# Kernel optimization log

Hardware: AMD Instinct MI355X
Metric: run time of the kernel (lower is better)

Reference implementation:

```python
import jax, jax.numpy as jnp
import numpy as np

NUM_HEADS = 8
NUM_NEIGHBORS = 32


def setup_inputs() -> dict:
    key = jax.random.key(0)
    ks = jax.random.split(key, 5)
    B, S, F, C = 4, 2048, 512, 3
    x = jax.random.normal(ks[0], (B, S, F), dtype=jnp.float32)
    coords = jax.random.uniform(ks[1], (B, S, C), dtype=jnp.float32)
    scale = 1.0 / np.sqrt(F)
    Wq = jax.random.normal(ks[2], (F, F), dtype=jnp.float32) * scale
    Wk = jax.random.normal(ks[3], (F, F), dtype=jnp.float32) * scale
    Wv = jax.random.normal(ks[4], (F, F), dtype=jnp.float32) * scale
    return {"x": x, "coords": coords, "Wq": Wq, "Wk": Wk, "Wv": Wv}


def _nearest_neighbors(coords, k):
    # coords: [B,S,C] -> dists [B,S,S]; drop self (index 0 after argsort)
    diff = coords[:, None, :, :] - coords[:, :, None, :]
    dists = jnp.linalg.norm(diff, axis=-1)
    return jnp.argsort(dists, axis=-1)[:, :, 1:k + 1]  # [B,S,K]


def reference(x, coords, Wq, Wk, Wv):
    B, S, F = x.shape
    H = NUM_HEADS
    D = F // H

    nn_idx = _nearest_neighbors(coords, NUM_NEIGHBORS)  # [B,S,K] int
    # dense boolean neighbor mask [B,S,S]: mask[b,q,kv] = kv in nn_idx[b,q]
    b_ix = jnp.arange(B)[:, None, None]
    q_ix = jnp.arange(S)[None, :, None]
    mask = jnp.zeros((B, S, S), dtype=bool).at[b_ix, q_ix, nn_idx].set(True)

    q = (x @ Wq.T).reshape(B, S, H, D).transpose(0, 2, 1, 3)  # [B,H,S,D]
    k = (x @ Wk.T).reshape(B, S, H, D).transpose(0, 2, 1, 3)
    v = (x @ Wv.T).reshape(B, S, H, D).transpose(0, 2, 1, 3)

    scale = 1.0 / jnp.sqrt(jnp.asarray(D, dtype=x.dtype))
    scores = jnp.einsum("bhqd,bhkd->bhqk", q, k) * scale
    neg_inf = jnp.asarray(-jnp.inf, dtype=scores.dtype)
    scores = jnp.where(mask[:, None, :, :], scores, neg_inf)
    attn = jax.nn.softmax(scores, axis=-1)
    out = jnp.einsum("bhqk,bhkd->bhqd", attn, v)  # [B,H,S,D]
    out = out.transpose(0, 2, 1, 3).reshape(B, S, F)
    metric = k.mean(axis=2)  # [B,H,D]
    return out, metric
```

## Files before the change

kernel.cpp:

```cpp
#include <hip/hip_runtime.h>
#include <stdint.h>

#define BATCH 4
#define SEQ   2048
#define FDIM  512
#define NHEAD 8
#define HDIM  64
#define KNN   32

typedef unsigned int u32;
typedef unsigned long long u64;
typedef unsigned short u16;
typedef unsigned short bf16_t;

typedef __attribute__((ext_vector_type(8))) short short8;
typedef __attribute__((ext_vector_type(4))) float f32x4;

#define SF  ((size_t)SEQ * FDIM)
#define BSF ((size_t)BATCH * SF)

#define CAST_NB 2432
#define XPART_NB 128

__device__ __forceinline__ bf16_t f2bf(float f) {
    u32 x = __float_as_uint(f);
    return (bf16_t)((x + 0x7FFFu + ((x >> 16) & 1u)) >> 16);
}
__device__ __forceinline__ float bf2f(bf16_t u) { return __uint_as_float(((u32)u) << 16); }
__device__ __forceinline__ void bf2x2(u32 p, float& a, float& b) {
    a = __uint_as_float(p << 16);
    b = __uint_as_float(p & 0xFFFF0000u);
}
__device__ __forceinline__ u64 min_u64(u64 a, u64 b) { return a < b ? a : b; }
__device__ __forceinline__ u64 shfl_xor_u64(u64 v, int m) {
    int lo = __shfl_xor((int)(u32)v, m, 64);
    int hi = __shfl_xor((int)(u32)(v >> 32), m, 64);
    return (((u64)(u32)hi) << 32) | (u32)lo;
}

__device__ __forceinline__ void cast_body(int cid,
                                          const float* __restrict__ x,
                                          const float* __restrict__ wq,
                                          const float* __restrict__ wk,
                                          const float* __restrict__ wv,
                                          bf16_t* __restrict__ xb,
                                          bf16_t* __restrict__ wqb,
                                          bf16_t* __restrict__ wkb,
                                          bf16_t* __restrict__ wvb) {
    int z, blk;
    if (cid < 2048) { z = 0; blk = cid; }
    else { int d = cid - 2048; z = 1 + (d >> 7); blk = d & 127; }
    const float* src = (z == 0) ? x : (z == 1) ? wq : (z == 2) ? wk : wv;
    bf16_t* dst      = (z == 0) ? xb : (z == 1) ? wqb : (z == 2) ? wkb : wvb;
    size_t idx = (size_t)blk * 256 + threadIdx.x;
    const float4 a = ((const float4*)src)[idx * 2 + 0];
    const float4 b = ((const float4*)src)[idx * 2 + 1];
    uint4 o;
    o.x = (u32)f2bf(a.x) | ((u32)f2bf(a.y) << 16);
    o.y = (u32)f2bf(a.z) | ((u32)f2bf(a.w) << 16);
    o.z = (u32)f2bf(b.x) | ((u32)f2bf(b.y) << 16);
    o.w = (u32)f2bf(b.z) | ((u32)f2bf(b.w) << 16);
    ((uint4*)dst)[idx] = o;
}

__device__ __forceinline__ void xpart_body(int id, const float* __restrict__ x,
                                           float* __restrict__ xpart) {
    const int b = id >> 5, chunk = id & 31;
    const int tid = threadIdx.x;
    const float* xp = x + (size_t)b * SF + (size_t)chunk * 64 * FDIM;
    float s0 = 0.f, s1 = 0.f;
    for (int r = 0; r < 64; ++r) {
        s0 += xp[(size_t)r * FDIM + tid];
        s1 += xp[(size_t)r * FDIM + tid + 256];
    }
    float* dst = xpart + (size_t)id * FDIM;
    dst[tid]       = s0 * (1.f / 2048.f);
    dst[tid + 256] = s1 * (1.f / 2048.f);
}

__device__ __forceinline__ void knn_body(char* smem, int blk,
                                         const float* __restrict__ coords,
                                         u16* __restrict__ nn_out) {
    u32* chist = (u32*)smem;
    u32* fhist = (u32*)(smem + 256);
    u64* bk    = (u64*)(smem + 1280);
    u64* wpart = (u64*)(smem + 1792);
    u32* sc    = (u32*)(smem + 1824);
    const int b   = blk >> 11;
    const int qi  = blk & (SEQ - 1);
    const int t   = threadIdx.x;
    const int wid = t >> 6, lane = t & 63;
    const size_t qb = (size_t)blk * KNN;

    fhist[t & 255] = 0;
    if (t < 64) chist[t] = 0;
    if (t == 0) { sc[2] = 0; sc[3] = 0; }

    const float* cb = coords + (size_t)b * SEQ * 3;
    const float qx = cb[qi * 3 + 0];
    const float qy = cb[qi * 3 + 1];
    const float qz = cb[qi * 3 + 2];

    float dist[8];
    int   ib[8];
    u64 tmin = ~0ull;
#pragma unroll
    for (int i = 0; i < 8; ++i) {
        int c = i * 256 + t;
        float dx = __fsub_rn(cb[c * 3 + 0], qx);
        float dy = __fsub_rn(cb[c * 3 + 1], qy);
        float dz = __fsub_rn(cb[c * 3 + 2], qz);
        float d2 = __fadd_rn(__fadd_rn(__fmul_rn(dx, dx), __fmul_rn(dy, dy)),
                             __fmul_rn(dz, dz));
        dist[i] = __fsqrt_rn(d2);
        ib[i] = (int)(dist[i] * 8192.0f);
        u64 key = (((u64)__float_as_uint(dist[i])) << 32) | (u32)c;
        tmin = min_u64(tmin, key);
    }
    tmin = min_u64(tmin, shfl_xor_u64(tmin, 1));
    tmin = min_u64(tmin, shfl_xor_u64(tmin, 2));
    tmin = min_u64(tmin, shfl_xor_u64(tmin, 4));
    tmin = min_u64(tmin, shfl_xor_u64(tmin, 8));
    tmin = min_u64(tmin, shfl_xor_u64(tmin, 16));
    tmin = min_u64(tmin, shfl_xor_u64(tmin, 32));
    if (lane == 0) wpart[wid] = tmin;
    __syncthreads();

#pragma unroll
    for (int i = 0; i < 8; ++i) atomicAdd(&chist[ib[i] >> 8], 1u);
    const u64 M = min_u64(min_u64(wpart[0], wpart[1]),
                          min_u64(wpart[2], wpart[3]));
    __syncthreads();

    if (t < 64) {
        u32 h = chist[t];
        u32 cum = h;
#pragma unroll
        for (int d = 1; d < 64; d <<= 1) {
            u32 v = (u32)__shfl_up((int)cum, d, 64);
            if (t >= d) cum += v;
        }
        u64 bal = __ballot(cum >= 33);
        int Bc = __ffsll((long long)bal) - 1;
        u32 excl = cum - h;
        u32 base = (u32)__shfl((int)excl, Bc, 64);
        if (t == 0) { sc[0] = (u32)Bc; sc[1] = base; }
    }
    __syncthreads();

    {
        const int Bc = (int)sc[0];
#pragma unroll
        for (int i = 0; i < 8; ++i)
            if ((ib[i] >> 8) == Bc) atomicAdd(&fhist[ib[i] & 255], 1u);
    }
    __syncthreads();

    if (t < 64) {
        const u32 Bc = sc[0], base = sc[1];
        u32 f0 = fhist[t * 4 + 0], f1 = fhist[t * 4 + 1];
        u32 f2 = fhist[t * 4 + 2], f3 = fhist[t * 4 + 3];
        u32 s = f0 + f1 + f2 + f3;
        u32 cum = s;
#pragma unroll
        for (int d = 1; d < 64; d <<= 1) {
            u32 v = (u32)__shfl_up((int)cum, d, 64);
            if (t >= d) cum += v;
        }
        u32 E = base + (cum - s);
        u32 c0 = E + f0, c1 = c0 + f1, c2 = c1 + f2, c3 = c2 + f3;
        u64 bal = __ballot(c3 >= 33);
        int L = __ffsll((long long)bal) - 1;
        if (t == L) {
            int j = (c0 >= 33) ? 0 : (c1 >= 33) ? 1 : (c2 >= 33) ? 2 : 3;
            sc[4] = (Bc << 8) | (u32)(t * 4 + j);
        }
    }
    __syncthreads();

    {
        const int ibt = (int)sc[4];
#pragma unroll
        for (int i = 0; i < 8; ++i) {
            int c = i * 256 + t;
            u64 key = (((u64)__float_as_uint(dist[i])) << 32) | (u32)c;
            if (ib[i] < ibt) {
                if (key != M) {
                    u32 pos = atomicAdd(&sc[2], 1u);
                    nn_out[qb + pos] = (u16)c;
                }
            } else if (ib[i] == ibt) {
                u32 bp = atomicAdd(&sc[3], 1u);
                if (bp < 64) bk[bp] = key;
            }
        }
    }
    __syncthreads();

    if (t < 64) {
        const u32 m = sc[2];
        const int n = (int)min(sc[3], 64u);
        const int need = 32 - (int)m;
        u64 k = (t < n) ? bk[t] : ~0ull;
        if (k == M) k = ~0ull;
#pragma unroll 1
        for (int r = 0; r < need; ++r) {
            u64 g = k;
            g = min_u64(g, shfl_xor_u64(g, 1));
            g = min_u64(g, shfl_xor_u64(g, 2));
            g = min_u64(g, shfl_xor_u64(g, 4));
            g = min_u64(g, shfl_xor_u64(g, 8));
            g = min_u64(g, shfl_xor_u64(g, 16));
            g = min_u64(g, shfl_xor_u64(g, 32));
            if (k == g) {
                nn_out[qb + m + r] = (u16)(g & 0x7FF);
                k = ~0ull;
            }
        }
    }
}

__global__ __launch_bounds__(256) void fused_ck(const float* __restrict__ x,
                                                const float* __restrict__ wq,
                                                const float* __restrict__ wk,
                                                const float* __restrict__ wv,
                                                bf16_t* __restrict__ xb,
                                                bf16_t* __restrict__ wqb,
                                                bf16_t* __restrict__ wkb,
                                                bf16_t* __restrict__ wvb,
                                                const float* __restrict__ coords,
                                                u16* __restrict__ nn_out,
                                                float* __restrict__ xpart) {
    __shared__ __align__(16) char smem[1856];
    const int bid = blockIdx.x;
    if (bid < CAST_NB) {
        cast_body(bid, x, wq, wk, wv, xb, wqb, wkb, wvb);
    } else if (bid < CAST_NB + XPART_NB) {
        xpart_body(bid - CAST_NB, x, xpart);
    } else {
        knn_body(smem, bid - CAST_NB - XPART_NB, coords, nn_out);
    }
}

__global__ __launch_bounds__(256) void gemm_mfma(const bf16_t* __restrict__ xb,
                                                 const bf16_t* __restrict__ wqb,
                                                 const bf16_t* __restrict__ wkb,
                                                 const bf16_t* __restrict__ wvb,
                                                 float* __restrict__ qout,
                                                 bf16_t* __restrict__ kvout,
                                                 const float* __restrict__ xpart,
                                                 const float* __restrict__ Wkf,
                                                 float* __restrict__ metric) {
    __shared__ __align__(16) bf16_t As[128 * 32];
    __shared__ __align__(16) bf16_t Bs[128 * 32];
    const int z = blockIdx.z;
    const int tid  = threadIdx.x;

    if (z == 3) {
        const int id = blockIdx.y * 4 + blockIdx.x;
        if (id >= 8) return;
        float* xbarL = (float*)As;
        const int b = id >> 1;
        float a0 = 0.f, a1 = 0.f;
#pragma unroll 4
        for (int c = 0; c < 32; ++c) {
            const float* xp = xpart + (size_t)((b << 5) | c) * FDIM;
            a0 += xp[tid];
            a1 += xp[tid + 256];
        }
        xbarL[tid] = a0; xbarL[tid + 256] = a1;
        __syncthreads();
        const int f = ((id & 1) << 8) | tid;
        const float* wr = Wkf + (size_t)f * FDIM;
        float acc = 0.f;
#pragma unroll 4
        for (int kk = 0; kk < FDIM; kk += 4) {
            float4 wv = *(const float4*)(wr + kk);
            acc += xbarL[kk + 0] * wv.x + xbarL[kk + 1] * wv.y
                 + xbarL[kk + 2] * wv.z + xbarL[kk + 3] * wv.w;
        }
        metric[(b << 9) | f] = acc;
        return;
    }

    const bf16_t* W = (z == 0) ? wqb : (z == 1) ? wkb : wvb;
    const int wid  = tid >> 6, lane = tid & 63;
    const int m16  = lane & 15, quad = lane >> 4;
    const int wm   = (wid & 1) * 64;
    const int wn   = (wid >> 1) * 64;
    const int m0   = blockIdx.y * 128;
    const int n0   = blockIdx.x * 128;

    const int sr = tid >> 2, sc = (tid & 3) * 8;
    const bf16_t* agp = xb + (size_t)(m0 + sr) * FDIM + sc;
    const bf16_t* bgp = W  + (size_t)(n0 + sr) * FDIM + sc;

    f32x4 acc[4][4];
#pragma unroll
    for (int i = 0; i < 4; ++i)
#pragma unroll
        for (int j = 0; j < 4; ++j) acc[i][j] = (f32x4){0.f, 0.f, 0.f, 0.f};

#pragma unroll 1
    for (int k0 = 0; k0 < FDIM; k0 += 32) {
        uint4 a0 = *(const uint4*)(agp + k0);
        uint4 a1 = *(const uint4*)(agp + (size_t)64 * FDIM + k0);
        uint4 b0 = *(const uint4*)(bgp + k0);
        uint4 b1 = *(const uint4*)(bgp + (size_t)64 * FDIM + k0);
        __syncthreads();
        *(uint4*)(As + sr * 32 + sc)        = a0;
        *(uint4*)(As + (sr + 64) * 32 + sc) = a1;
        *(uint4*)(Bs + sr * 32 + sc)        = b0;
        *(uint4*)(Bs + (sr + 64) * 32 + sc) = b1;
        __syncthreads();

        short8 af[4], bfr[4];
#pragma unroll
        for (int i = 0; i < 4; ++i)
            af[i] = *(const short8*)(As + (wm + i * 16 + m16) * 32 + quad * 8);
#pragma unroll
        for (int j = 0; j < 4; ++j)
            bfr[j] = *(const short8*)(Bs + (wn + j * 16 + m16) * 32 + quad * 8);
#pragma unroll
        for (int i = 0; i < 4; ++i)
#pragma unroll
            for (int j = 0; j < 4; ++j)
                acc[i][j] = __builtin_amdgcn_mfma_f32_16x16x32_bf16(af[i], bfr[j],
                                                                    acc[i][j], 0, 0, 0);
    }

    if (z == 0) {
#pragma unroll
        for (int i = 0; i < 4; ++i) {
            const int rowb = m0 + wm + i * 16 + quad * 4;
#pragma unroll
            for (int r = 0; r < 4; ++r) {
                float* orow = qout + (size_t)(rowb + r) * FDIM + n0 + wn + m16;
                orow[ 0] = acc[i][0][r]; orow[16] = acc[i][1][r];
                orow[32] = acc[i][2][r]; orow[48] = acc[i][3][r];
            }
        }
    } else {
        bf16_t* base = kvout + (size_t)(z - 1) * BSF;
#pragma unroll
        for (int i = 0; i < 4; ++i) {
            const int rowb = m0 + wm + i * 16 + quad * 4;
#pragma unroll
            for (int r = 0; r < 4; ++r) {
                bf16_t* orow = base + (size_t)(rowb + r) * FDIM + n0 + wn + m16;
                orow[ 0] = f2bf(acc[i][0][r]); orow[16] = f2bf(acc[i][1][r]);
                orow[32] = f2bf(acc[i][2][r]); orow[48] = f2bf(acc[i][3][r]);
            }
        }
    }
}

__global__ __launch_bounds__(256, 8) void attn_kernel(const bf16_t* __restrict__ kv,
                                                      const u16* __restrict__ nn,
                                                      float* __restrict__ out) {
    __shared__ float qsl[4][64];
    const int i   = blockIdx.x;
    const int b   = (i & 7) >> 1;
    const int jb  = ((i >> 3) << 1) | (i & 1);
    const int tid = threadIdx.x;
    const int wid = tid >> 6, lane = tid & 63;
    const int gid = (jb << 2) | wid;
    const int qi  = gid >> 3, h = gid & 7;
    const int blk = (b << 11) | qi;

    int sreg = 0;
    if (lane < KNN) sreg = (int)nn[(size_t)blk * KNN + lane] & (SEQ - 1);
    qsl[wid][lane] = out[(size_t)blk * FDIM + h * HDIM + lane];
    __asm__ volatile("s_waitcnt lgkmcnt(0)" ::: "memory");
    __builtin_amdgcn_wave_barrier();

    const int j = lane & 31, half = lane >> 5;
    const int rowj = __shfl(sreg, j, 64);
    const bf16_t* kreg = kv + ((size_t)((b << 11) + rowj)) * FDIM + h * HDIM + half * 32;
    uint4 k0 = *(const uint4*)(kreg + 0);
    uint4 k1 = *(const uint4*)(kreg + 8);
    uint4 k2 = *(const uint4*)(kreg + 16);
    uint4 k3 = *(const uint4*)(kreg + 24);

    const int g = lane >> 4, l = lane & 15;
    const bf16_t* vbase = kv + BSF + ((size_t)(b << 11)) * FDIM + h * HDIM + l * 4;
    uint2 vv[8];
#pragma unroll
    for (int t2 = 0; t2 < 8; ++t2) {
        const int row = __shfl(sreg, (g << 3) | t2, 64);
        vv[t2] = *(const uint2*)(vbase + (size_t)row * FDIM);
    }

    const float* qp = &qsl[wid][half * 32];
    float acc = 0.f;
    {
        float f0, f1, f2, f3, f4, f5, f6, f7;
        bf2x2(k0.x, f0, f1); bf2x2(k0.y, f2, f3);
        bf2x2(k0.z, f4, f5); bf2x2(k0.w, f6, f7);
        acc += qp[0] * f0 + qp[1] * f1 + qp[2] * f2 + qp[3] * f3
             + qp[4] * f4 + qp[5] * f5 + qp[6] * f6 + qp[7] * f7;
        bf2x2(k1.x, f0, f1); bf2x2(k1.y, f2, f3);
        bf2x2(k1.z, f4, f5); bf2x2(k1.w, f6, f7);
        acc += qp[8] * f0 + qp[9] * f1 + qp[10] * f2 + qp[11] * f3
             + qp[12] * f4 + qp[13] * f5 + qp[14] * f6 + qp[15] * f7;
        bf2x2(k2.x, f0, f1); bf2x2(k2.y, f2, f3);
        bf2x2(k2.z, f4, f5); bf2x2(k2.w, f6, f7);
        acc += qp[16] * f0 + qp[17] * f1 + qp[18] * f2 + qp[19] * f3
             + qp[20] * f4 + qp[21] * f5 + qp[22] * f6 + qp[23] * f7;
        bf2x2(k3.x, f0, f1); bf2x2(k3.y, f2, f3);
        bf2x2(k3.z, f4, f5); bf2x2(k3.w, f6, f7);
        acc += qp[24] * f0 + qp[25] * f1 + qp[26] * f2 + qp[27] * f3
             + qp[28] * f4 + qp[29] * f5 + qp[30] * f6 + qp[31] * f7;
    }
    acc += __shfl_xor(acc, 32, 64);
    float s = acc * 0.125f;
    float m = s;
    m = fmaxf(m, __shfl_xor(m, 1, 64));
    m = fmaxf(m, __shfl_xor(m, 2, 64));
    m = fmaxf(m, __shfl_xor(m, 4, 64));
    m = fmaxf(m, __shfl_xor(m, 8, 64));
    m = fmaxf(m, __shfl_xor(m, 16, 64));
    float e = __expf(s - m);
    float sum = e;
    sum += __shfl_xor(sum, 1, 64);
    sum += __shfl_xor(sum, 2, 64);
    sum += __shfl_xor(sum, 4, 64);
    sum += __shfl_xor(sum, 8, 64);
    sum += __shfl_xor(sum, 16, 64);
    float w = e / sum;

    float o0 = 0.f, o1 = 0.f, o2 = 0.f, o3 = 0.f;
#pragma unroll
    for (int t2 = 0; t2 < 8; ++t2) {
        const float wj = __shfl(w, (g << 3) | t2, 64);
        float f0, f1, f2, f3;
        bf2x2(vv[t2].x, f0, f1); bf2x2(vv[t2].y, f2, f3);
        o0 += wj * f0; o1 += wj * f1; o2 += wj * f2; o3 += wj * f3;
    }
    o0 += __shfl_xor(o0, 16, 64); o0 += __shfl_xor(o0, 32, 64);
    o1 += __shfl_xor(o1, 16, 64); o1 += __shfl_xor(o1, 32, 64);
    o2 += __shfl_xor(o2, 16, 64); o2 += __shfl_xor(o2, 32, 64);
    o3 += __shfl_xor(o3, 16, 64); o3 += __shfl_xor(o3, 32, 64);
    if (g == 0) {
        float4 ov = make_float4(o0, o1, o2, o3);
        *(float4*)(out + (size_t)blk * FDIM + h * HDIM + l * 4) = ov;
    }
}

extern "C" void kernel_launch(void* const* d_in, const int* in_sizes, int n_in,
                              void* d_out, int out_size, void* d_ws, size_t ws_size,
                              hipStream_t stream) {
    const float* x      = (const float*)d_in[0];
    const float* coords = (const float*)d_in[1];
    const float* Wq     = (const float*)d_in[2];
    const float* Wk     = (const float*)d_in[3];
    const float* Wv     = (const float*)d_in[4];
    float* out    = (float*)d_out;
    float* metric = out + BSF;

    char* p = (char*)d_ws;
    bf16_t* xb    = (bf16_t*)p;                      p += BSF * sizeof(bf16_t);
    bf16_t* wqb   = (bf16_t*)p;                      p += (size_t)FDIM * FDIM * sizeof(bf16_t);
    bf16_t* wkb   = (bf16_t*)p;                      p += (size_t)FDIM * FDIM * sizeof(bf16_t);
    bf16_t* wvb   = (bf16_t*)p;                      p += (size_t)FDIM * FDIM * sizeof(bf16_t);
    bf16_t* kv    = (bf16_t*)p;                      p += 2 * BSF * sizeof(bf16_t);
    u16*    nn    = (u16*)p;                         p += (size_t)BATCH * SEQ * KNN * sizeof(u16);
    float*  xpart = (float*)p;

    fused_ck<<<CAST_NB + XPART_NB + BATCH * SEQ, 256, 0, stream>>>(
        x, Wq, Wk, Wv, xb, wqb, wkb, wvb, coords, nn, xpart);

    gemm_mfma<<<dim3(FDIM / 128, (BATCH * SEQ) / 128, 4), 256, 0, stream>>>(
        xb, wqb, wkb, wvb, out, kv, xpart, Wk, metric);

    attn_kernel<<<BATCH * SEQ * NHEAD / 4, 256, 0, stream>>>(kv, nn, out);
}
```

Measured before the change: 184.3 us.

## Store Q as bf16 and use packed bf16 dot2 plus DPP reductions in attention

The projection epilogue now writes Q as bf16 into the fp32 output buffer, laid out with a per-head stride so each head's 64 values sit in the first half of its slot. The attention kernel loads Q as packed u32 pairs and computes QK dot products with the fdot2 bf16 builtin in two accumulator chains. It also replaces the intra-16-lane shuffles in the softmax max and sum reductions with DPP row operations. This lowers Q write/read traffic and ALU work, but Q is rounded to bf16 and the reduction depends on the DPP control codes being correct.

New measurement: 189.7 us. +2.9%, slower.

```diff
diff --git a/kernel.cpp b/kernel.cpp
--- a/kernel.cpp
+++ b/kernel.cpp
@@ -15,6 +15,7 @@
 
 typedef __attribute__((ext_vector_type(8))) short short8;
 typedef __attribute__((ext_vector_type(4))) float f32x4;
+typedef __attribute__((ext_vector_type(2))) __bf16 bf16x2;
 
 #define SF  ((size_t)SEQ * FDIM)
 #define BSF ((size_t)BATCH * SF)
@@ -36,6 +37,23 @@
     int lo = __shfl_xor((int)(u32)v, m, 64);
     int hi = __shfl_xor((int)(u32)(v >> 32), m, 64);
     return (((u64)(u32)hi) << 32) | (u32)lo;
+}
+
+__device__ __forceinline__ float dot2bf(u32 a, u32 b, float c) {
+#if __has_builtin(__builtin_amdgcn_fdot2_f32_bf16)
+    return __builtin_amdgcn_fdot2_f32_bf16(__builtin_bit_cast(bf16x2, a),
+                                           __builtin_bit_cast(bf16x2, b), c, false);
+#else
+    float a0, a1, b0, b1;
+    bf2x2(a, a0, a1); bf2x2(b, b0, b1);
+    return c + a0 * b0 + a1 * b1;
+#endif
+}
+
+template <int CTRL>
+__device__ __forceinline__ float dppf(float x) {
+    return __int_as_float(__builtin_amdgcn_update_dpp(
+        0, __float_as_int(x), CTRL, 0xF, 0xF, true));
 }
 
 __device__ __forceinline__ void cast_body(int cid,
@@ -330,14 +348,18 @@
     }
 
     if (z == 0) {
+        u16* qb16 = (u16*)qout;
 #pragma unroll
         for (int i = 0; i < 4; ++i) {
             const int rowb = m0 + wm + i * 16 + quad * 4;
 #pragma unroll
             for (int r = 0; r < 4; ++r) {
-                float* orow = qout + (size_t)(rowb + r) * FDIM + n0 + wn + m16;
-                orow[ 0] = acc[i][0][r]; orow[16] = acc[i][1][r];
-                orow[32] = acc[i][2][r]; orow[48] = acc[i][3][r];
+                u16* orow = qb16 + (size_t)(rowb + r) * (2 * FDIM);
+#pragma unroll
+                for (int jj = 0; jj < 4; ++jj) {
+                    const int col = n0 + wn + m16 + jj * 16;
+                    orow[((col >> 6) << 7) + (col & 63)] = f2bf(acc[i][jj][r]);
+                }
             }
         }
     } else {
@@ -358,7 +380,7 @@
 __global__ __launch_bounds__(256, 8) void attn_kernel(const bf16_t* __restrict__ kv,
                                                       const u16* __restrict__ nn,
                                                       float* __restrict__ out) {
-    __shared__ float qsl[4][64];
+    __shared__ __align__(16) u32 qslu[4][32];
     const int i   = blockIdx.x;
     const int b   = (i & 7) >> 1;
     const int jb  = ((i >> 3) << 1) | (i & 1);
@@ -369,8 +391,10 @@
     const int blk = (b << 11) | qi;
 
     int sreg = 0;
-    if (lane < KNN) sreg = (int)nn[(size_t)blk * KNN + lane] & (SEQ - 1);
-    qsl[wid][lane] = out[(size_t)blk * FDIM + h * HDIM + lane];
+    if (lane < 32) {
+        sreg = (int)nn[(size_t)blk * KNN + lane] & (SEQ - 1);
+        qslu[wid][lane] = ((const u32*)out)[(size_t)blk * FDIM + h * HDIM + lane];
+    }
     __asm__ volatile("s_waitcnt lgkmcnt(0)" ::: "memory");
     __builtin_amdgcn_wave_barrier();
 
@@ -391,41 +415,32 @@
         vv[t2] = *(const uint2*)(vbase + (size_t)row * FDIM);
     }
 
-    const float* qp = &qsl[wid][half * 32];
-    float acc = 0.f;
-    {
-        float f0, f1, f2, f3, f4, f5, f6, f7;
-        bf2x2(k0.x, f0, f1); bf2x2(k0.y, f2, f3);
-        bf2x2(k0.z, f4, f5); bf2x2(k0.w, f6, f7);
-        acc += qp[0] * f0 + qp[1] * f1 + qp[2] * f2 + qp[3] * f3
-             + qp[4] * f4 + qp[5] * f5 + qp[6] * f6 + qp[7] * f7;
-        bf2x2(k1.x, f0, f1); bf2x2(k1.y, f2, f3);
-        bf2x2(k1.z, f4, f5); bf2x2(k1.w, f6, f7);
-        acc += qp[8] * f0 + qp[9] * f1 + qp[10] * f2 + qp[11] * f3
-             + qp[12] * f4 + qp[13] * f5 + qp[14] * f6 + qp[15] * f7;
-        bf2x2(k2.x, f0, f1); bf2x2(k2.y, f2, f3);
-        bf2x2(k2.z, f4, f5); bf2x2(k2.w, f6, f7);
-        acc += qp[16] * f0 + qp[17] * f1 + qp[18] * f2 + qp[19] * f3
-             + qp[20] * f4 + qp[21] * f5 + qp[22] * f6 + qp[23] * f7;
-        bf2x2(k3.x, f0, f1); bf2x2(k3.y, f2, f3);
-        bf2x2(k3.z, f4, f5); bf2x2(k3.w, f6, f7);
-        acc += qp[24] * f0 + qp[25] * f1 + qp[26] * f2 + qp[27] * f3
-             + qp[28] * f4 + qp[29] * f5 + qp[30] * f6 + qp[31] * f7;
-    }
+    const u32* qp = &qslu[wid][half * 16];
+    float a0 = 0.f, a1 = 0.f;
+    a0 = dot2bf(qp[0],  k0.x, a0); a1 = dot2bf(qp[1],  k0.y, a1);
+    a0 = dot2bf(qp[2],  k0.z, a0); a1 = dot2bf(qp[3],  k0.w, a1);
+    a0 = dot2bf(qp[4],  k1.x, a0); a1 = dot2bf(qp[5],  k1.y, a1);
+    a0 = dot2bf(qp[6],  k1.z, a0); a1 = dot2bf(qp[7],  k1.w, a1);
+    a0 = dot2bf(qp[8],  k2.x, a0); a1 = dot2bf(qp[9],  k2.y, a1);
+    a0 = dot2bf(qp[10], k2.z, a0); a1 = dot2bf(qp[11], k2.w, a1);
+    a0 = dot2bf(qp[12], k3.x, a0); a1 = dot2bf(qp[13], k3.y, a1);
+    a0 = dot2bf(qp[14], k3.z, a0); a1 = dot2bf(qp[15], k3.w, a1);
+    float acc = a0 + a1;
     acc += __shfl_xor(acc, 32, 64);
     float s = acc * 0.125f;
+
     float m = s;
-    m = fmaxf(m, __shfl_xor(m, 1, 64));
-    m = fmaxf(m, __shfl_xor(m, 2, 64));
-    m = fmaxf(m, __shfl_xor(m, 4, 64));
-    m = fmaxf(m, __shfl_xor(m, 8, 64));
+    m = fmaxf(m, dppf<0xB1>(m));
+    m = fmaxf(m, dppf<0x4E>(m));
+    m = fmaxf(m, dppf<0x141>(m));
+    m = fmaxf(m, dppf<0x140>(m));
     m = fmaxf(m, __shfl_xor(m, 16, 64));
     float e = __expf(s - m);
     float sum = e;
-    sum += __shfl_xor(sum, 1, 64);
-    sum += __shfl_xor(sum, 2, 64);
-    sum += __shfl_xor(sum, 4, 64);
-    sum += __shfl_xor(sum, 8, 64);
+    sum += dppf<0xB1>(sum);
+    sum += dppf<0x4E>(sum);
+    sum += dppf<0x141>(sum);
+    sum += dppf<0x140>(sum);
     sum += __shfl_xor(sum, 16, 64);
     float w = e / sum;
 
```

## Remap attention lanes to 8-lane groups with DPP reductions and LDS output sum

Applied to the files above, without the earlier changes.

Rearranges the per-(query,head) attention wave so each lane holds 8 contiguous dims of 4 neighbors for both K and V, loaded as 16-byte vectors issued together up front. Dot-product partials are reduced with DPP row operations instead of a cross-half shuffle, and softmax max/sum use fewer shuffles. The output is reduced across the 8 neighbor groups through a shared-memory buffer instead of shuffle trees. In exchange it uses more LDS and registers, and the occupancy hint drops from 8 to 6.

New measurement: 163.0 us. 11.5% less time.

```diff
diff --git a/kernel.cpp b/kernel.cpp
--- a/kernel.cpp
+++ b/kernel.cpp
@@ -36,6 +36,28 @@
     int lo = __shfl_xor((int)(u32)v, m, 64);
     int hi = __shfl_xor((int)(u32)(v >> 32), m, 64);
     return (((u64)(u32)hi) << 32) | (u32)lo;
+}
+
+template <int CTRL>
+__device__ __forceinline__ float dppf(float x) {
+    return __int_as_float(__builtin_amdgcn_update_dpp(
+        0, __float_as_int(x), CTRL, 0xF, 0xF, true));
+}
+
+__device__ __forceinline__ float dot8(uint4 k, f32x4 qa, f32x4 qb) {
+    float f0, f1, f2, f3, f4, f5, f6, f7;
+    bf2x2(k.x, f0, f1); bf2x2(k.y, f2, f3);
+    bf2x2(k.z, f4, f5); bf2x2(k.w, f6, f7);
+    return qa.x * f0 + qa.y * f1 + qa.z * f2 + qa.w * f3
+         + qb.x * f4 + qb.y * f5 + qb.z * f6 + qb.w * f7;
+}
+
+__device__ __forceinline__ void acc8(uint4 v, float w, float* o) {
+    float f0, f1, f2, f3, f4, f5, f6, f7;
+    bf2x2(v.x, f0, f1); bf2x2(v.y, f2, f3);
+    bf2x2(v.z, f4, f5); bf2x2(v.w, f6, f7);
+    o[0] += w * f0; o[1] += w * f1; o[2] += w * f2; o[3] += w * f3;
+    o[4] += w * f4; o[5] += w * f5; o[6] += w * f6; o[7] += w * f7;
 }
 
 __device__ __forceinline__ void cast_body(int cid,
@@ -355,10 +377,11 @@
     }
 }
 
-__global__ __launch_bounds__(256, 8) void attn_kernel(const bf16_t* __restrict__ kv,
+__global__ __launch_bounds__(256, 6) void attn_kernel(const bf16_t* __restrict__ kv,
                                                       const u16* __restrict__ nn,
                                                       float* __restrict__ out) {
     __shared__ float qsl[4][64];
+    __shared__ float osl[4][8][64];
     const int i   = blockIdx.x;
     const int b   = (i & 7) >> 1;
     const int jb  = ((i >> 3) << 1) | (i & 1);
@@ -371,80 +394,65 @@
     int sreg = 0;
     if (lane < KNN) sreg = (int)nn[(size_t)blk * KNN + lane] & (SEQ - 1);
     qsl[wid][lane] = out[(size_t)blk * FDIM + h * HDIM + lane];
+
+    const int g3 = lane >> 3, l8 = lane & 7;
+    const int r0 = __shfl(sreg,      g3, 64);
+    const int r1 = __shfl(sreg,  8 + g3, 64);
+    const int r2 = __shfl(sreg, 16 + g3, 64);
+    const int r3 = __shfl(sreg, 24 + g3, 64);
+
+    const bf16_t* base = kv + ((size_t)(b << 11)) * FDIM + h * HDIM + l8 * 8;
+    const uint4 k0 = *(const uint4*)(base + (size_t)r0 * FDIM);
+    const uint4 k1 = *(const uint4*)(base + (size_t)r1 * FDIM);
+    const uint4 k2 = *(const uint4*)(base + (size_t)r2 * FDIM);
+    const uint4 k3 = *(const uint4*)(base + (size_t)r3 * FDIM);
+    const uint4 v0 = *(const uint4*)(base + BSF + (size_t)r0 * FDIM);
+    const uint4 v1 = *(const uint4*)(base + BSF + (size_t)r1 * FDIM);
+    const uint4 v2 = *(const uint4*)(base + BSF + (size_t)r2 * FDIM);
+    const uint4 v3 = *(const uint4*)(base + BSF + (size_t)r3 * FDIM);
+
     __asm__ volatile("s_waitcnt lgkmcnt(0)" ::: "memory");
     __builtin_amdgcn_wave_barrier();
-
-    const int j = lane & 31, half = lane >> 5;
-    const int rowj = __shfl(sreg, j, 64);
-    const bf16_t* kreg = kv + ((size_t)((b << 11) + rowj)) * FDIM + h * HDIM + half * 32;
-    uint4 k0 = *(const uint4*)(kreg + 0);
-    uint4 k1 = *(const uint4*)(kreg + 8);
-    uint4 k2 = *(const uint4*)(kreg + 16);
-    uint4 k3 = *(const uint4*)(kreg + 24);
-
-    const int g = lane >> 4, l = lane & 15;
-    const bf16_t* vbase = kv + BSF + ((size_t)(b << 11)) * FDIM + h * HDIM + l * 4;
-    uint2 vv[8];
-#pragma unroll
-    for (int t2 = 0; t2 < 8; ++t2) {
-        const int row = __shfl(sreg, (g << 3) | t2, 64);
-        vv[t2] = *(const uint2*)(vbase + (size_t)row * FDIM);
-    }
-
-    const float* qp = &qsl[wid][half * 32];
-    float acc = 0.f;
-    {
-        float f0, f1, f2, f3, f4, f5, f6, f7;
-        bf2x2(k0.x, f0, f1); bf2x2(k0.y, f2, f3);
-        bf2x2(k0.z, f4, f5); bf2x2(k0.w, f6, f7);
-        acc += qp[0] * f0 + qp[1] * f1 + qp[2] * f2 + qp[3] * f3
-             + qp[4] * f4 + qp[5] * f5 + qp[6] * f6 + qp[7] * f7;
-        bf2x2(k1.x, f0, f1); bf2x2(k1.y, f2, f3);
-        bf2x2(k1.z, f4, f5); bf2x2(k1.w, f6, f7);
-        acc += qp[8] * f0 + qp[9] * f1 + qp[10] * f2 + qp[11] * f3
-             + qp[12] * f4 + qp[13] * f5 + qp[14] * f6 + qp[15] * f7;
-        bf2x2(k2.x, f0, f1); bf2x2(k2.y, f2, f3);
-        bf2x2(k2.z, f4, f5); bf2x2(k2.w, f6, f7);
-        acc += qp[16] * f0 + qp[17] * f1 + qp[18] * f2 + qp[19] * f3
-             + qp[20] * f4 + qp[21] * f5 + qp[22] * f6 + qp[23] * f7;
-        bf2x2(k3.x, f0, f1); bf2x2(k3.y, f2, f3);
-        bf2x2(k3.z, f4, f5); bf2x2(k3.w, f6, f7);
-        acc += qp[24] * f0 + qp[25] * f1 + qp[26] * f2 + qp[27] * f3
-             + qp[28] * f4 + qp[29] * f5 + qp[30] * f6 + qp[31] * f7;
-    }
-    acc += __shfl_xor(acc, 32, 64);
-    float s = acc * 0.125f;
-    float m = s;
-    m = fmaxf(m, __shfl_xor(m, 1, 64));
-    m = fmaxf(m, __shfl_xor(m, 2, 64));
-    m = fmaxf(m, __shfl_xor(m, 4, 64));
-    m = fmaxf(m, __shfl_xor(m, 8, 64));
-    m = fmaxf(m, __shfl_xor(m, 16, 64));
-    float e = __expf(s - m);
-    float sum = e;
-    sum += __shfl_xor(sum, 1, 64);
-    sum += __shfl_xor(sum, 2, 64);
-    sum += __shfl_xor(sum, 4, 64);
-    sum += __shfl_xor(sum, 8, 64);
-    sum += __shfl_xor(sum, 16, 64);
-    float w = e / sum;
-
-    float o0 = 0.f, o1 = 0.f, o2 = 0.f, o3 = 0.f;
-#pragma unroll
-    for (int t2 = 0; t2 < 8; ++t2) {
-        const float wj = __shfl(w, (g << 3) | t2, 64);
-        float f0, f1, f2, f3;
-        bf2x2(vv[t2].x, f0, f1); bf2x2(vv[t2].y, f2, f3);
-        o0 += wj * f0; o1 += wj * f1; o2 += wj * f2; o3 += wj * f3;
-    }
-    o0 += __shfl_xor(o0, 16, 64); o0 += __shfl_xor(o0, 32, 64);
-    o1 += __shfl_xor(o1, 16, 64); o1 += __shfl_xor(o1, 32, 64);
-    o2 += __shfl_xor(o2, 16, 64); o2 += __shfl_xor(o2, 32, 64);
-    o3 += __shfl_xor(o3, 16, 64); o3 += __shfl_xor(o3, 32, 64);
-    if (g == 0) {
-        float4 ov = make_float4(o0, o1, o2, o3);
-        *(float4*)(out + (size_t)blk * FDIM + h * HDIM + l * 4) = ov;
-    }
+    const f32x4 qa = *(const f32x4*)&qsl[wid][l8 * 8];
+    const f32x4 qb = *(const f32x4*)&qsl[wid][l8 * 8 + 4];
+
+    float s0 = dot8(k0, qa, qb);
+    float s1 = dot8(k1, qa, qb);
+    float s2 = dot8(k2, qa, qb);
+    float s3 = dot8(k3, qa, qb);
+    s0 += dppf<0xB1>(s0); s0 += dppf<0x4E>(s0); s0 += dppf<0x141>(s0);
+    s1 += dppf<0xB1>(s1); s1 += dppf<0x4E>(s1); s1 += dppf<0x141>(s1);
+    s2 += dppf<0xB1>(s2); s2 += dppf<0x4E>(s2); s2 += dppf<0x141>(s2);
+    s3 += dppf<0xB1>(s3); s3 += dppf<0x4E>(s3); s3 += dppf<0x141>(s3);
+    s0 *= 0.125f; s1 *= 0.125f; s2 *= 0.125f; s3 *= 0.125f;
+
+    float ml = fmaxf(fmaxf(s0, s1), fmaxf(s2, s3));
+    ml = fmaxf(ml, dppf<0x140>(ml));
+    ml = fmaxf(ml, __shfl_xor(ml, 16, 64));
+    ml = fmaxf(ml, __shfl_xor(ml, 32, 64));
+    const float e0 = __expf(s0 - ml), e1 = __expf(s1 - ml);
+    const float e2 = __expf(s2 - ml), e3 = __expf(s3 - ml);
+    float sl = (e0 + e1) + (e2 + e3);
+    sl += dppf<0x140>(sl);
+    sl += __shfl_xor(sl, 16, 64);
+    sl += __shfl_xor(sl, 32, 64);
+    const float rs = 1.0f / sl;
+    const float w0 = e0 * rs, w1 = e1 * rs, w2 = e2 * rs, w3 = e3 * rs;
+
+    float o[8] = {0.f, 0.f, 0.f, 0.f, 0.f, 0.f, 0.f, 0.f};
+    acc8(v0, w0, o);
+    acc8(v1, w1, o);
+    acc8(v2, w2, o);
+    acc8(v3, w3, o);
+
+    *(f32x4*)&osl[wid][g3][l8 * 8]     = (f32x4){o[0], o[1], o[2], o[3]};
+    *(f32x4*)&osl[wid][g3][l8 * 8 + 4] = (f32x4){o[4], o[5], o[6], o[7]};
+    __asm__ volatile("s_waitcnt lgkmcnt(0)" ::: "memory");
+    __builtin_amdgcn_wave_barrier();
+    float r = osl[wid][0][lane];
+#pragma unroll
+    for (int g = 1; g < 8; ++g) r += osl[wid][g][lane];
+    out[(size_t)blk * FDIM + h * HDIM + lane] = r;
 }
 
 extern "C" void kernel_launch(void* const* d_in, const int* in_sizes, int n_in,
```
